# Optimization experiments

Measured on AMD Instinct MI355X. Metric: run time of the kernel, lower is better.

## Reference

```python
import jax, jax.numpy as jnp
import numpy as np
import math

QDIM = 512
KDIM = 512
MID = 512
MAIN_N = 2048
OTHER_N = 2048
BATCH = 32
NEG_BIG = -float(1 << 32)


def setup_inputs() -> dict:
    key = jax.random.key(0)
    ks = jax.random.split(key, 8)
    main_feat = jax.random.normal(ks[0], (MAIN_N, QDIM), dtype=jnp.float32)
    other_feat = jax.random.normal(ks[1], (OTHER_N, KDIM), dtype=jnp.float32)
    fix_feat = jax.random.uniform(ks[2], (BATCH, OTHER_N), dtype=jnp.float32)
    mask = jax.random.randint(ks[3], (MAIN_N, OTHER_N), 0, 2).astype(bool)
    # Linear params (PyTorch layout: W [out, in], b [out])
    sq = 1.0 / math.sqrt(QDIM)
    sk = 1.0 / math.sqrt(KDIM)
    Wq = jax.random.uniform(ks[4], (MID, QDIM), jnp.float32, -sq, sq)
    bq = jax.random.uniform(ks[5], (MID,), jnp.float32, -sq, sq)
    Wk = jax.random.uniform(ks[6], (MID, KDIM), jnp.float32, -sk, sk)
    bk = jax.random.uniform(ks[7], (MID,), jnp.float32, -sk, sk)
    return {"main_feat": main_feat, "other_feat": other_feat, "fix_feat": fix_feat,
            "mask": mask, "Wq": Wq, "bq": bq, "Wk": Wk, "bk": bk}


def reference(main_feat, other_feat, fix_feat, mask, Wq, bq, Wk, bk):
    # Q: [main, mid], K: [other, mid]
    Q = main_feat @ Wq.T + bq
    K = other_feat @ Wk.T + bk
    attn = (Q @ K.T) / math.sqrt(MID)            # [main, other]
    attn = jnp.where(mask, NEG_BIG, attn)
    attn = jax.nn.softmax(attn, axis=-1)
    # diag_embed(fix_feat) @ other_feat == per-token broadcast scale
    scaled = fix_feat[:, :, None] * other_feat[None, :, :]   # [batch, other, Kdim]
    return jnp.einsum('mo,bok->bmk', attn, scaled)           # [batch, main, Kdim]
```

## Files before the change

### kernel.cpp

```cpp
#include <hip/hip_runtime.h>
#include <hip/hip_bf16.h>

typedef unsigned short u16;
typedef __attribute__((ext_vector_type(8))) short short8;
typedef __attribute__((ext_vector_type(4))) float f32x4;

#define BATCH_ 32

static __device__ __forceinline__ float b2f(u16 u) {
  union { unsigned int i; float f; } v; v.i = ((unsigned int)u) << 16; return v.f;
}
static __device__ __forceinline__ u16 f2b(float x) {
  unsigned int i = __float_as_uint(x);
  unsigned int r = (i + 0x7fffu + ((i >> 16) & 1u)) >> 16;
  return (u16)r;
}

#define GCAST(p) ((const __attribute__((address_space(1))) void*)(p))
#define LCAST(p) ((__attribute__((address_space(3))) void*)(p))

__global__ __launch_bounds__(256) void cvt_bf16(const float* __restrict__ src,
                                                u16* __restrict__ dst, int n) {
  int i = (blockIdx.x * 256 + threadIdx.x) * 4;
  if (i >= n) return;
  float4 v = *(const float4*)(src + i);
  ushort4 o;
  o.x = f2b(v.x); o.y = f2b(v.y); o.z = f2b(v.z); o.w = f2b(v.w);
  *(ushort4*)(dst + i) = o;
}

__global__ __launch_bounds__(256) void transpose_cvt(const float* __restrict__ src,
                                                     u16* __restrict__ dst, int R, int C) {
  __shared__ float tile[32][33];
  int c0 = blockIdx.x * 32, r0 = blockIdx.y * 32;
  int tx = threadIdx.x & 31, ty = threadIdx.x >> 5;
  #pragma unroll
  for (int i = 0; i < 32; i += 8)
    tile[ty + i][tx] = src[(long long)(r0 + ty + i) * C + c0 + tx];
  __syncthreads();
  #pragma unroll
  for (int i = 0; i < 32; i += 8)
    dst[(long long)(c0 + ty + i) * R + r0 + tx] = f2b(tile[tx][ty + i]);
}

__global__ __launch_bounds__(256) void build_scaled(const u16* __restrict__ oT,
                                                    const float* __restrict__ fix,
                                                    u16* __restrict__ out) {
  long long i4 = (long long)blockIdx.x * 256 + threadIdx.x;
  int o = (int)(i4 & 511) * 4;
  long long bk = i4 >> 9;
  int b = (int)(bk >> 9);
  int kk = (int)(bk & 511);
  ushort4 v = *(const ushort4*)(oT + (long long)kk * 2048 + o);
  float4 f = *(const float4*)(fix + (long long)b * 2048 + o);
  ushort4 r;
  r.x = f2b(b2f(v.x) * f.x); r.y = f2b(b2f(v.y) * f.y);
  r.z = f2b(b2f(v.z) * f.z); r.w = f2b(b2f(v.w) * f.w);
  *(ushort4*)(out + bk * 2048 + o) = r;
}

__global__ __launch_bounds__(256) void softmax_mask(const float* __restrict__ S,
                                                    const int* __restrict__ mask,
                                                    u16* __restrict__ P, int N) {
  const float scale = 0.044194173824159216f;
  int row = blockIdx.x;
  int t = threadIdx.x;
  long long base = (long long)row * N;
  float vals[8]; int msk[8];
  float mx = -3.0e38f;
  #pragma unroll
  for (int i = 0; i < 8; ++i) {
    int c = t + i * 256;
    float s = S[base + c] * scale;
    int m = mask[base + c];
    vals[i] = s; msk[i] = m;
    if (!m) mx = fmaxf(mx, s);
  }
  #pragma unroll
  for (int off = 32; off; off >>= 1) mx = fmaxf(mx, __shfl_xor(mx, off));
  __shared__ float sred[4];
  if ((t & 63) == 0) sred[t >> 6] = mx;
  __syncthreads();
  mx = fmaxf(fmaxf(sred[0], sred[1]), fmaxf(sred[2], sred[3]));
  __syncthreads();
  float e[8]; float sum = 0.f;
  #pragma unroll
  for (int i = 0; i < 8; ++i) {
    e[i] = msk[i] ? 0.f : __expf(vals[i] - mx);
    sum += e[i];
  }
  #pragma unroll
  for (int off = 32; off; off >>= 1) sum += __shfl_xor(sum, off);
  if ((t & 63) == 0) sred[t >> 6] = sum;
  __syncthreads();
  sum = sred[0] + sred[1] + sred[2] + sred[3];
  float inv = (sum > 0.f) ? (1.f / sum) : 0.f;
  #pragma unroll
  for (int i = 0; i < 8; ++i) {
    int c = t + i * 256;
    P[base + c] = f2b(e[i] * inv);
  }
}

#define GBM 128
#define GBN 128
#define GBK 32

template<int EPI>
__global__ __launch_bounds__(256) void gemm_lds(
    const u16* __restrict__ A, const u16* __restrict__ Bt,
    const float* __restrict__ bias,
    const u16* __restrict__ Bt2, const float* __restrict__ bias2,
    float* __restrict__ outF, u16* __restrict__ outB,
    int M, int N, int K) {
  __shared__ u16 sA[GBM * GBK];
  __shared__ u16 sB[GBN * GBK];
  int m0 = blockIdx.y * GBM, n0 = blockIdx.x * GBN;
  if (EPI == 0) {
    if (2 * blockIdx.y >= gridDim.y) { Bt = Bt2; bias = bias2; }
  }
  int t = threadIdx.x;
  int wid = t >> 6, lane = t & 63;
  int wm = (wid >> 1) * 64, wn = (wid & 1) * 64;
  int lr = lane & 15, lq = lane >> 4;
  int srow = lane >> 2, schunk = (lane & 3) * 8;

  f32x4 acc[4][4];
  #pragma unroll
  for (int i = 0; i < 4; ++i)
    #pragma unroll
    for (int j = 0; j < 4; ++j)
      acc[i][j] = (f32x4){0.f, 0.f, 0.f, 0.f};

  const u16* gA = A + (long long)(m0 + wid * 32 + srow) * K + schunk;
  const u16* gB = Bt + (long long)(n0 + wid * 32 + srow) * K + schunk;
  u16* lA = &sA[(wid * 32) * GBK];
  u16* lB = &sB[(wid * 32) * GBK];
  const long long rowskip = (long long)16 * K;

  for (int k0 = 0; k0 < K; k0 += GBK) {
    __builtin_amdgcn_global_load_lds(GCAST(gA + k0),           LCAST(lA),            16, 0, 0);
    __builtin_amdgcn_global_load_lds(GCAST(gA + k0 + rowskip), LCAST(lA + 16 * GBK), 16, 0, 0);
    __builtin_amdgcn_global_load_lds(GCAST(gB + k0),           LCAST(lB),            16, 0, 0);
    __builtin_amdgcn_global_load_lds(GCAST(gB + k0 + rowskip), LCAST(lB + 16 * GBK), 16, 0, 0);
    __syncthreads();
    short8 af[4], bf[4];
    #pragma unroll
    for (int i = 0; i < 4; ++i)
      af[i] = *(const short8*)&sA[(wm + i * 16 + lr) * GBK + lq * 8];
    #pragma unroll
    for (int j = 0; j < 4; ++j)
      bf[j] = *(const short8*)&sB[(wn + j * 16 + lr) * GBK + lq * 8];
    #pragma unroll
    for (int i = 0; i < 4; ++i)
      #pragma unroll
      for (int j = 0; j < 4; ++j)
        acc[i][j] = __builtin_amdgcn_mfma_f32_16x16x32_bf16(af[i], bf[j], acc[i][j], 0, 0, 0);
    __syncthreads();
  }

  #pragma unroll
  for (int i = 0; i < 4; ++i) {
    #pragma unroll
    for (int j = 0; j < 4; ++j) {
      int col = n0 + wn + j * 16 + lr;
      #pragma unroll
      for (int r = 0; r < 4; ++r) {
        int row = m0 + wm + i * 16 + lq * 4 + r;
        float v = acc[i][j][r];
        if (EPI == 0) {
          outB[(long long)row * N + col] = f2b(v + bias[col]);
        } else {
          outF[(long long)row * N + col] = v;
        }
      }
    }
  }
}

__global__ __launch_bounds__(512, 2) void gemm_ring(
    const u16* __restrict__ A, const u16* __restrict__ Bt,
    float* __restrict__ outF, int M, int N, int K) {
  __shared__ u16 lds[4][2][8192];

  int nwg = gridDim.x * gridDim.y;
  int wg = blockIdx.y * gridDim.x + blockIdx.x;
  int cpx = nwg >> 3;
  int swz = (wg & 7) * cpx + (wg >> 3);
  int bx = swz & 7, by = swz >> 3;
  int m0 = bx * 256, n0 = by * 256;

  int t = threadIdx.x;
  int w = t >> 6, lane = t & 63;
  int wr = w >> 2, wc = w & 3;
  int lr = lane & 15, lq = lane >> 4;
  int csw = (((lr >> 1) & 3) ^ lq) * 8;

  int srow = t >> 2;
  int sgc = (((srow >> 1) & 3) ^ (t & 3)) * 8;
  const u16* pA0 = A + (long long)(m0 + srow) * K + sgc;
  const u16* pA1 = pA0 + (long long)128 * K;
  const u16* pB0 = Bt + (long long)(n0 + srow) * K + sgc;
  const u16* pB1 = pB0 + (long long)128 * K;
  const int lbase = (w * 16) * 32;

  f32x4 acc[8][4];
  #pragma unroll
  for (int i = 0; i < 8; ++i)
    #pragma unroll
    for (int j = 0; j < 4; ++j)
      acc[i][j] = (f32x4){0.f, 0.f, 0.f, 0.f};

  const int NT = K >> 5;

  #define STAGE_TILE(KT, SB)                                                          \
    do {                                                                              \
      long long cofs = (long long)(KT) * 32;                                          \
      __builtin_amdgcn_global_load_lds(GCAST(pA0 + cofs), LCAST(&lds[SB][0][lbase]),           16, 0, 0); \
      __builtin_amdgcn_global_load_lds(GCAST(pA1 + cofs), LCAST(&lds[SB][0][lbase + 128 * 32]), 16, 0, 0); \
      __builtin_amdgcn_global_load_lds(GCAST(pB0 + cofs), LCAST(&lds[SB][1][lbase]),           16, 0, 0); \
      __builtin_amdgcn_global_load_lds(GCAST(pB1 + cofs), LCAST(&lds[SB][1][lbase + 128 * 32]), 16, 0, 0); \
    } while (0)

  STAGE_TILE(0, 0);
  STAGE_TILE(1, 1);
  STAGE_TILE(2, 2);
  asm volatile("s_waitcnt vmcnt(8)" ::: "memory");
  __builtin_amdgcn_s_barrier();
  __builtin_amdgcn_sched_barrier(0);

  for (int kt = 0; kt < NT; ++kt) {
    const int buf = kt & 3;
    short8 af[8], bf[4];
    #pragma unroll
    for (int i = 0; i < 8; ++i)
      af[i] = *(const short8*)&lds[buf][0][(wr * 128 + i * 16 + lr) * 32 + csw];
    #pragma unroll
    for (int j = 0; j < 4; ++j)
      bf[j] = *(const short8*)&lds[buf][1][(wc * 64 + j * 16 + lr) * 32 + csw];

    if (kt + 3 < NT) STAGE_TILE(kt + 3, (kt + 3) & 3);

    __builtin_amdgcn_sched_barrier(0);
    __builtin_amdgcn_s_barrier();
    asm volatile("s_waitcnt lgkmcnt(0)" ::: "memory");
    __builtin_amdgcn_sched_barrier(0);

    __builtin_amdgcn_s_setprio(1);
    #pragma unroll
    for (int i = 0; i < 8; ++i)
      #pragma unroll
      for (int j = 0; j < 4; ++j)
        acc[i][j] = __builtin_amdgcn_mfma_f32_16x16x32_bf16(af[i], bf[j], acc[i][j], 0, 0, 0);
    __builtin_amdgcn_s_setprio(0);

    if (kt + 3 < NT)       asm volatile("s_waitcnt vmcnt(8)" ::: "memory");
    else if (kt == NT - 3) asm volatile("s_waitcnt vmcnt(4)" ::: "memory");
    else if (kt == NT - 2) asm volatile("s_waitcnt vmcnt(0)" ::: "memory");
    __builtin_amdgcn_s_barrier();
    __builtin_amdgcn_sched_barrier(0);
  }
  #undef STAGE_TILE

  #pragma unroll
  for (int i = 0; i < 8; ++i) {
    #pragma unroll
    for (int j = 0; j < 4; ++j) {
      int col = n0 + wc * 64 + j * 16 + lr;
      int b = col >> 9, kc = col & 511;
      float* ob = outF + (long long)b * ((long long)M * 512) + kc;
      #pragma unroll
      for (int r = 0; r < 4; ++r) {
        int row = m0 + wr * 128 + i * 16 + lq * 4 + r;
        ob[(long long)row * 512] = acc[i][j][r];
      }
    }
  }
}

#define BMT 128
#define BNT 128
#define BKT 32
#define LDSP 40

template<int MODE>
__global__ __launch_bounds__(256) void gemm_bt(
    const u16* __restrict__ A, const u16* __restrict__ Bt,
    const float* __restrict__ bias, const float* __restrict__ fixmat,
    float* __restrict__ outF, u16* __restrict__ outB,
    int M, int N, int K, long long out_batch_stride, int bt_batch_stride) {
  __shared__ u16 sA[BMT][LDSP];
  __shared__ u16 sB[BNT][LDSP];
  int b = blockIdx.z;
  const u16* Bt_b = Bt + (long long)b * bt_batch_stride;
  const float* fixrow = (MODE == 2) ? (fixmat + (long long)b * K) : nullptr;
  float* out_b = (MODE != 0) ? (outF + (long long)b * out_batch_stride) : nullptr;

  int m0 = blockIdx.y * BMT, n0 = blockIdx.x * BNT;
  int t = threadIdx.x;
  int wid = t >> 6, lane = t & 63;
  int wm = (wid >> 1) * 64, wn = (wid & 1) * 64;
  int lr = lane & 15, lq = lane >> 4;

  f32x4 acc[4][4];
  #pragma unroll
  for (int i = 0; i < 4; ++i)
    #pragma unroll
    for (int j = 0; j < 4; ++j)
      acc[i][j] = (f32x4){0.f, 0.f, 0.f, 0.f};

  int srow = t >> 1, scg = (t & 1) * 16;

  for (int k0 = 0; k0 < K; k0 += BKT) {
    {
      const u16* src = A + (long long)(m0 + srow) * K + k0 + scg;
      short8 v0 = *(const short8*)(src);
      short8 v1 = *(const short8*)(src + 8);
      *(short8*)&sA[srow][scg] = v0;
      *(short8*)&sA[srow][scg + 8] = v1;
    }
    {
      const u16* src = Bt_b + (long long)(n0 + srow) * K + k0 + scg;
      short8 v0 = *(const short8*)(src);
      short8 v1 = *(const short8*)(src + 8);
      if (MODE == 2) {
        u16* p0 = (u16*)&v0; u16* p1 = (u16*)&v1;
        #pragma unroll
        for (int j = 0; j < 8; ++j) {
          p0[j] = f2b(b2f(p0[j]) * fixrow[k0 + scg + j]);
          p1[j] = f2b(b2f(p1[j]) * fixrow[k0 + scg + 8 + j]);
        }
      }
      *(short8*)&sB[srow][scg] = v0;
      *(short8*)&sB[srow][scg + 8] = v1;
    }
    __syncthreads();
    short8 af[4], bf[4];
    #pragma unroll
    for (int i = 0; i < 4; ++i)
      af[i] = *(const short8*)&sA[wm + i * 16 + lr][lq * 8];
    #pragma unroll
    for (int j = 0; j < 4; ++j)
      bf[j] = *(const short8*)&sB[wn + j * 16 + lr][lq * 8];
    #pragma unroll
    for (int i = 0; i < 4; ++i)
      #pragma unroll
      for (int j = 0; j < 4; ++j)
        acc[i][j] = __builtin_amdgcn_mfma_f32_16x16x32_bf16(af[i], bf[j], acc[i][j], 0, 0, 0);
    __syncthreads();
  }

  #pragma unroll
  for (int i = 0; i < 4; ++i) {
    #pragma unroll
    for (int j = 0; j < 4; ++j) {
      int col = n0 + wn + j * 16 + lr;
      #pragma unroll
      for (int r = 0; r < 4; ++r) {
        int row = m0 + wm + i * 16 + lq * 4 + r;
        float v = acc[i][j][r];
        if (MODE == 0) {
          v += bias[col];
          outB[(long long)row * N + col] = f2b(v);
        } else {
          out_b[(long long)row * N + col] = v;
        }
      }
    }
  }
}

extern "C" void kernel_launch(void* const* d_in, const int* in_sizes, int n_in,
                              void* d_out, int out_size, void* d_ws, size_t ws_size,
                              hipStream_t stream) {
  const float* main_feat  = (const float*)d_in[0];
  const float* other_feat = (const float*)d_in[1];
  const float* fix_feat   = (const float*)d_in[2];
  const int*   mask       = (const int*)d_in[3];
  const float* Wq         = (const float*)d_in[4];
  const float* bq         = (const float*)d_in[5];
  const float* Wk         = (const float*)d_in[6];
  const float* bk         = (const float*)d_in[7];
  float* out = (float*)d_out;

  char* ws = (char*)d_ws;
  const size_t OFF_MAINB  = 0;
  const size_t OFF_OTHERB = 2097152;
  const size_t OFF_WQB    = 4194304;
  const size_t OFF_WKB    = 4718592;
  const size_t OFF_QB     = 5242880;
  const size_t OFF_KB     = 7340032;
  const size_t OFF_OTB    = 9437184;
  const size_t OFF_P      = 11534336;
  const size_t OFF_S      = 19922944;
  const size_t OFF_SCALED = 36700160;
  const size_t NEED_SCALED = OFF_SCALED + (size_t)BATCH_ * 512 * 2048 * 2;

  u16* mainB  = (u16*)(ws + OFF_MAINB);
  u16* otherB = (u16*)(ws + OFF_OTHERB);
  u16* WqB    = (u16*)(ws + OFF_WQB);
  u16* WkB    = (u16*)(ws + OFF_WKB);
  u16* QB     = (u16*)(ws + OFF_QB);
  u16* KB     = (u16*)(ws + OFF_KB);
  u16* oTB    = (u16*)(ws + OFF_OTB);
  u16* P      = (u16*)(ws + OFF_P);
  float* S    = (float*)(ws + OFF_S);
  u16* scaled = (u16*)(ws + OFF_SCALED);
  bool use_scaled = (ws_size >= NEED_SCALED);

  cvt_bf16<<<1024, 256, 0, stream>>>(main_feat, mainB, 2048 * 512);
  cvt_bf16<<<1024, 256, 0, stream>>>(other_feat, otherB, 2048 * 512);
  cvt_bf16<<<256, 256, 0, stream>>>(Wq, WqB, 512 * 512);
  cvt_bf16<<<256, 256, 0, stream>>>(Wk, WkB, 512 * 512);
  transpose_cvt<<<dim3(16, 64), 256, 0, stream>>>(other_feat, oTB, 2048, 512);

  if (use_scaled) {
    gemm_lds<0><<<dim3(4, 32), 256, 0, stream>>>(mainB, WqB, bq, WkB, bk,
        nullptr, QB, 4096, 512, 512);
    gemm_lds<1><<<dim3(16, 16), 256, 0, stream>>>(QB, KB, nullptr, nullptr, nullptr,
        S, nullptr, 2048, 2048, 512);
    softmax_mask<<<2048, 256, 0, stream>>>(S, mask, P, 2048);
    build_scaled<<<32768, 256, 0, stream>>>(oTB, fix_feat, scaled);
    gemm_ring<<<dim3(8, 64), 512, 0, stream>>>(P, scaled, out, 2048, 16384, 2048);
  } else {
    gemm_bt<0><<<dim3(4, 16, 1), 256, 0, stream>>>(mainB, WqB, bq, nullptr,
        nullptr, QB, 2048, 512, 512, 0, 0);
    gemm_bt<0><<<dim3(4, 16, 1), 256, 0, stream>>>(otherB, WkB, bk, nullptr,
        nullptr, KB, 2048, 512, 512, 0, 0);
    gemm_bt<1><<<dim3(16, 16, 1), 256, 0, stream>>>(QB, KB, nullptr, nullptr,
        S, nullptr, 2048, 2048, 512, 0, 0);
    softmax_mask<<<2048, 256, 0, stream>>>(S, mask, P, 2048);
    gemm_bt<2><<<dim3(4, 16, BATCH_), 256, 0, stream>>>(P, oTB, nullptr, fix_feat,
        out, nullptr, 2048, 512, 2048, 1048576LL, 0);
  }
}
```

Measured before the change: 197.0 us.

## Double-buffer register fragments to overlap LDS reads with MFMA in GEMM loop

Restructures the main GEMM k-loop into a two-step unrolled software pipeline. Fragments for the next tile are read from LDS into a second register set while MFMAs run on the current set, and the wait on global loads is tightened to one tile in flight. This targets the LDS-read latency that previously sat in front of every MFMA block, at the cost of doubling fragment registers (which may lower occupancy or cause spills) and adding explicit prologue/epilogue code that assumes NT is at least 4 and even.

```diff
diff --git a/kernel.cpp b/kernel.cpp
--- a/kernel.cpp
+++ b/kernel.cpp
@@ -216,51 +216,81 @@
   #define STAGE_TILE(KT, SB)                                                          \
     do {                                                                              \
       long long cofs = (long long)(KT) * 32;                                          \
-      __builtin_amdgcn_global_load_lds(GCAST(pA0 + cofs), LCAST(&lds[SB][0][lbase]),           16, 0, 0); \
+      __builtin_amdgcn_global_load_lds(GCAST(pA0 + cofs), LCAST(&lds[SB][0][lbase]),            16, 0, 0); \
       __builtin_amdgcn_global_load_lds(GCAST(pA1 + cofs), LCAST(&lds[SB][0][lbase + 128 * 32]), 16, 0, 0); \
-      __builtin_amdgcn_global_load_lds(GCAST(pB0 + cofs), LCAST(&lds[SB][1][lbase]),           16, 0, 0); \
+      __builtin_amdgcn_global_load_lds(GCAST(pB0 + cofs), LCAST(&lds[SB][1][lbase]),            16, 0, 0); \
       __builtin_amdgcn_global_load_lds(GCAST(pB1 + cofs), LCAST(&lds[SB][1][lbase + 128 * 32]), 16, 0, 0); \
     } while (0)
+
+  #define RD_FRAGS(AF, BF, BUF) {                                                     \
+    _Pragma("unroll")                                                                 \
+    for (int i = 0; i < 8; ++i)                                                       \
+      AF[i] = *(const short8*)&lds[BUF][0][(wr * 128 + i * 16 + lr) * 32 + csw];      \
+    _Pragma("unroll")                                                                 \
+    for (int j = 0; j < 4; ++j)                                                       \
+      BF[j] = *(const short8*)&lds[BUF][1][(wc * 64 + j * 16 + lr) * 32 + csw]; }
+
+  #define MFMA_BLK(AF, BF) {                                                          \
+    __builtin_amdgcn_s_setprio(1);                                                    \
+    _Pragma("unroll")                                                                 \
+    for (int i = 0; i < 8; ++i)                                                       \
+      _Pragma("unroll")                                                               \
+      for (int j = 0; j < 4; ++j)                                                     \
+        acc[i][j] = __builtin_amdgcn_mfma_f32_16x16x32_bf16(AF[i], BF[j], acc[i][j], 0, 0, 0); \
+    __builtin_amdgcn_s_setprio(0); }
+
+  short8 afA[8], bfA[4], afB[8], bfB[4];
 
   STAGE_TILE(0, 0);
   STAGE_TILE(1, 1);
   STAGE_TILE(2, 2);
-  asm volatile("s_waitcnt vmcnt(8)" ::: "memory");
+  asm volatile("s_waitcnt vmcnt(4)" ::: "memory");
   __builtin_amdgcn_s_barrier();
   __builtin_amdgcn_sched_barrier(0);
-
-  for (int kt = 0; kt < NT; ++kt) {
-    const int buf = kt & 3;
-    short8 af[8], bf[4];
-    #pragma unroll
-    for (int i = 0; i < 8; ++i)
-      af[i] = *(const short8*)&lds[buf][0][(wr * 128 + i * 16 + lr) * 32 + csw];
-    #pragma unroll
-    for (int j = 0; j < 4; ++j)
-      bf[j] = *(const short8*)&lds[buf][1][(wc * 64 + j * 16 + lr) * 32 + csw];
-
-    if (kt + 3 < NT) STAGE_TILE(kt + 3, (kt + 3) & 3);
-
-    __builtin_amdgcn_sched_barrier(0);
+  RD_FRAGS(afA, bfA, 0);
+
+  for (int kt = 0; kt + 4 < NT; kt += 2) {
+    RD_FRAGS(afB, bfB, ((kt + 1) & 3));
+    STAGE_TILE(kt + 3, ((kt + 3) & 3));
+    __builtin_amdgcn_sched_barrier(0);
+    MFMA_BLK(afA, bfA);
+    __builtin_amdgcn_sched_barrier(0);
+    asm volatile("s_waitcnt vmcnt(4)" ::: "memory");
     __builtin_amdgcn_s_barrier();
-    asm volatile("s_waitcnt lgkmcnt(0)" ::: "memory");
-    __builtin_amdgcn_sched_barrier(0);
-
-    __builtin_amdgcn_s_setprio(1);
-    #pragma unroll
-    for (int i = 0; i < 8; ++i)
-      #pragma unroll
-      for (int j = 0; j < 4; ++j)
-        acc[i][j] = __builtin_amdgcn_mfma_f32_16x16x32_bf16(af[i], bf[j], acc[i][j], 0, 0, 0);
-    __builtin_amdgcn_s_setprio(0);
-
-    if (kt + 3 < NT)       asm volatile("s_waitcnt vmcnt(8)" ::: "memory");
-    else if (kt == NT - 3) asm volatile("s_waitcnt vmcnt(4)" ::: "memory");
-    else if (kt == NT - 2) asm volatile("s_waitcnt vmcnt(0)" ::: "memory");
+    __builtin_amdgcn_sched_barrier(0);
+    RD_FRAGS(afA, bfA, ((kt + 2) & 3));
+    STAGE_TILE(kt + 4, ((kt + 4) & 3));
+    __builtin_amdgcn_sched_barrier(0);
+    MFMA_BLK(afB, bfB);
+    __builtin_amdgcn_sched_barrier(0);
+    asm volatile("s_waitcnt vmcnt(4)" ::: "memory");
     __builtin_amdgcn_s_barrier();
     __builtin_amdgcn_sched_barrier(0);
   }
+
+  RD_FRAGS(afB, bfB, ((NT - 3) & 3));
+  STAGE_TILE(NT - 1, ((NT - 1) & 3));
+  __builtin_amdgcn_sched_barrier(0);
+  MFMA_BLK(afA, bfA);
+  __builtin_amdgcn_sched_barrier(0);
+  asm volatile("s_waitcnt vmcnt(4)" ::: "memory");
+  __builtin_amdgcn_s_barrier();
+  __builtin_amdgcn_sched_barrier(0);
+  RD_FRAGS(afA, bfA, ((NT - 2) & 3));
+  __builtin_amdgcn_sched_barrier(0);
+  MFMA_BLK(afB, bfB);
+  __builtin_amdgcn_sched_barrier(0);
+  asm volatile("s_waitcnt vmcnt(0)" ::: "memory");
+  __builtin_amdgcn_s_barrier();
+  __builtin_amdgcn_sched_barrier(0);
+  RD_FRAGS(afB, bfB, ((NT - 1) & 3));
+  __builtin_amdgcn_sched_barrier(0);
+  MFMA_BLK(afA, bfA);
+  MFMA_BLK(afB, bfB);
+
   #undef STAGE_TILE
+  #undef RD_FRAGS
+  #undef MFMA_BLK
 
   #pragma unroll
   for (int i = 0; i < 8; ++i) {
```

Result: faster. 190.8 us (-3.2%).

## Restructure ring GEMM into double-buffered BK=64 tiles with four interleaved phases

Applied to the files above, without the earlier changes.

The big GEMM kernel moves from a 4-deep ring of K=32 tiles to a double buffer of K=64 tiles. Each iteration is split into four phases, and each phase interleaves LDS fragment reads, part of the next tile's global-to-LDS loads, and a 4x4 MFMA block. The LDS swizzle changes to an 8-way XOR on 64-wide rows. The aim is to halve the loop trip count and overlap loads with MFMA at a finer grain. In exchange it adds more barriers per iteration, waits on vmcnt(0) every iteration, and keeps only one tile of prefetch depth.

```diff
diff --git a/kernel.cpp b/kernel.cpp
--- a/kernel.cpp
+++ b/kernel.cpp
@@ -181,7 +181,7 @@
 __global__ __launch_bounds__(512, 2) void gemm_ring(
     const u16* __restrict__ A, const u16* __restrict__ Bt,
     float* __restrict__ outF, int M, int N, int K) {
-  __shared__ u16 lds[4][2][8192];
+  __shared__ u16 lds[2 * 32768];
 
   int nwg = gridDim.x * gridDim.y;
   int wg = blockIdx.y * gridDim.x + blockIdx.x;
@@ -194,15 +194,18 @@
   int w = t >> 6, lane = t & 63;
   int wr = w >> 2, wc = w & 3;
   int lr = lane & 15, lq = lane >> 4;
-  int csw = (((lr >> 1) & 3) ^ lq) * 8;
-
-  int srow = t >> 2;
-  int sgc = (((srow >> 1) & 3) ^ (t & 3)) * 8;
-  const u16* pA0 = A + (long long)(m0 + srow) * K + sgc;
-  const u16* pA1 = pA0 + (long long)128 * K;
-  const u16* pB0 = Bt + (long long)(n0 + srow) * K + sgc;
-  const u16* pB1 = pB0 + (long long)128 * K;
-  const int lbase = (w * 16) * 32;
+
+  const int s0 = ((lq) ^ (lr & 7)) * 8;
+  const int s1 = ((4 + lq) ^ (lr & 7)) * 8;
+  const int arow = wr * 128 + lr;
+  const int brow = wc * 64 + lr;
+
+  int sr = t >> 3;
+  int sch = ((t & 7) ^ (sr & 7)) * 8;
+  const u16* pA = A + (long long)(m0 + sr) * K + sch;
+  const u16* pB = Bt + (long long)(n0 + sr) * K + sch;
+  const int ldst = (t >> 6) * 512;
+  const long long rsk = (long long)64 * K;
 
   f32x4 acc[8][4];
   #pragma unroll
@@ -211,56 +214,85 @@
     for (int j = 0; j < 4; ++j)
       acc[i][j] = (f32x4){0.f, 0.f, 0.f, 0.f};
 
-  const int NT = K >> 5;
-
-  #define STAGE_TILE(KT, SB)                                                          \
-    do {                                                                              \
-      long long cofs = (long long)(KT) * 32;                                          \
-      __builtin_amdgcn_global_load_lds(GCAST(pA0 + cofs), LCAST(&lds[SB][0][lbase]),           16, 0, 0); \
-      __builtin_amdgcn_global_load_lds(GCAST(pA1 + cofs), LCAST(&lds[SB][0][lbase + 128 * 32]), 16, 0, 0); \
-      __builtin_amdgcn_global_load_lds(GCAST(pB0 + cofs), LCAST(&lds[SB][1][lbase]),           16, 0, 0); \
-      __builtin_amdgcn_global_load_lds(GCAST(pB1 + cofs), LCAST(&lds[SB][1][lbase + 128 * 32]), 16, 0, 0); \
-    } while (0)
-
-  STAGE_TILE(0, 0);
-  STAGE_TILE(1, 1);
-  STAGE_TILE(2, 2);
-  asm volatile("s_waitcnt vmcnt(8)" ::: "memory");
+  const int NT = K >> 6;
+
+  #define STG(OP, C, KT, NB)                                                          \
+    __builtin_amdgcn_global_load_lds(                                                 \
+      GCAST(((OP) ? pB : pA) + (long long)(C) * rsk + (long long)(KT) * 64),          \
+      LCAST(&lds[(NB) * 32768 + (OP) * 16384 + (C) * 4096 + ldst]), 16, 0, 0)
+
+  #define RDA(DST, IB, SH, BUF) {                                                     \
+    _Pragma("unroll")                                                                 \
+    for (int ii = 0; ii < 4; ++ii)                                                    \
+      DST[ii] = *(const short8*)&lds[(BUF) * 32768 + (arow + ((IB) + ii) * 16) * 64 + (SH)]; }
+
+  #define RDB(DST, SH, BUF) {                                                         \
+    _Pragma("unroll")                                                                 \
+    for (int jj = 0; jj < 4; ++jj)                                                    \
+      DST[jj] = *(const short8*)&lds[(BUF) * 32768 + 16384 + (brow + jj * 16) * 64 + (SH)]; }
+
+  #define MF16(AF, BF, IB) {                                                          \
+    __builtin_amdgcn_s_setprio(1);                                                    \
+    _Pragma("unroll")                                                                 \
+    for (int ii = 0; ii < 4; ++ii)                                                    \
+      _Pragma("unroll")                                                               \
+      for (int jj = 0; jj < 4; ++jj)                                                  \
+        acc[(IB) + ii][jj] =                                                          \
+          __builtin_amdgcn_mfma_f32_16x16x32_bf16(AF[ii], BF[jj], acc[(IB) + ii][jj], 0, 0, 0); \
+    __builtin_amdgcn_s_setprio(0); }
+
+  #define PH_SYNC() do {                                                              \
+    __builtin_amdgcn_sched_barrier(0);                                                \
+    __builtin_amdgcn_s_barrier();                                                     \
+    asm volatile("s_waitcnt lgkmcnt(0)" ::: "memory");                                \
+    __builtin_amdgcn_sched_barrier(0);                                                \
+  } while (0)
+
+  short8 aA[4], aB[4], aC[4], aD[4], b0[4], b1[4];
+
+  #pragma unroll
+  for (int c = 0; c < 4; ++c) { STG(0, c, 0, 0); STG(1, c, 0, 0); }
+  asm volatile("s_waitcnt vmcnt(0)" ::: "memory");
   __builtin_amdgcn_s_barrier();
   __builtin_amdgcn_sched_barrier(0);
 
   for (int kt = 0; kt < NT; ++kt) {
-    const int buf = kt & 3;
-    short8 af[8], bf[4];
-    #pragma unroll
-    for (int i = 0; i < 8; ++i)
-      af[i] = *(const short8*)&lds[buf][0][(wr * 128 + i * 16 + lr) * 32 + csw];
-    #pragma unroll
-    for (int j = 0; j < 4; ++j)
-      bf[j] = *(const short8*)&lds[buf][1][(wc * 64 + j * 16 + lr) * 32 + csw];
-
-    if (kt + 3 < NT) STAGE_TILE(kt + 3, (kt + 3) & 3);
-
+    const int buf = kt & 1, nb = buf ^ 1;
+    const int st = (kt + 1 < NT);
+    RDA(aA, 0, s0, buf); RDB(b0, s0, buf);
+    if (st) { STG(0, 0, kt + 1, nb); STG(0, 1, kt + 1, nb); }
+    PH_SYNC();
+    MF16(aA, b0, 0);
     __builtin_amdgcn_sched_barrier(0);
     __builtin_amdgcn_s_barrier();
-    asm volatile("s_waitcnt lgkmcnt(0)" ::: "memory");
-    __builtin_amdgcn_sched_barrier(0);
-
-    __builtin_amdgcn_s_setprio(1);
-    #pragma unroll
-    for (int i = 0; i < 8; ++i)
-      #pragma unroll
-      for (int j = 0; j < 4; ++j)
-        acc[i][j] = __builtin_amdgcn_mfma_f32_16x16x32_bf16(af[i], bf[j], acc[i][j], 0, 0, 0);
-    __builtin_amdgcn_s_setprio(0);
-
-    if (kt + 3 < NT)       asm volatile("s_waitcnt vmcnt(8)" ::: "memory");
-    else if (kt == NT - 3) asm volatile("s_waitcnt vmcnt(4)" ::: "memory");
-    else if (kt == NT - 2) asm volatile("s_waitcnt vmcnt(0)" ::: "memory");
+    RDA(aB, 4, s0, buf); RDB(b1, s1, buf);
+    if (st) { STG(0, 2, kt + 1, nb); STG(0, 3, kt + 1, nb); }
+    PH_SYNC();
+    MF16(aB, b0, 4);
+    __builtin_amdgcn_sched_barrier(0);
     __builtin_amdgcn_s_barrier();
-    __builtin_amdgcn_sched_barrier(0);
-  }
-  #undef STAGE_TILE
+    RDA(aC, 0, s1, buf); RDA(aD, 4, s1, buf);
+    if (st) { STG(1, 0, kt + 1, nb); STG(1, 1, kt + 1, nb); }
+    PH_SYNC();
+    MF16(aC, b1, 0);
+    __builtin_amdgcn_sched_barrier(0);
+    __builtin_amdgcn_s_barrier();
+    if (st) { STG(1, 2, kt + 1, nb); STG(1, 3, kt + 1, nb); }
+    __builtin_amdgcn_sched_barrier(0);
+    __builtin_amdgcn_s_barrier();
+    __builtin_amdgcn_sched_barrier(0);
+    MF16(aD, b1, 4);
+    __builtin_amdgcn_sched_barrier(0);
+    asm volatile("s_waitcnt vmcnt(0)" ::: "memory");
+    __builtin_amdgcn_s_barrier();
+    __builtin_amdgcn_sched_barrier(0);
+  }
+
+  #undef STG
+  #undef RDA
+  #undef RDB
+  #undef MF16
+  #undef PH_SYNC
 
   #pragma unroll
   for (int i = 0; i < 8; ++i) {
```

Measured after the change: 201.2 us. 1.02x slower.
